# Optimization experiments

Hardware: AMD Instinct MI355X
Metric: run time of the kernel (lower is better)

Reference implementation:

```python
import jax, jax.numpy as jnp
import numpy as np

B, S, D, H, FF = 4, 1024, 1024, 16, 4096
DH = D // H
EPS = 1e-5  # torch LayerNorm default


def _layernorm(x, g, b):
    m = jnp.mean(x, axis=-1, keepdims=True)
    v = jnp.mean((x - m) ** 2, axis=-1, keepdims=True)
    return (x - m) * jax.lax.rsqrt(v + EPS) * g + b


def setup_inputs() -> dict:
    key = jax.random.key(0)
    ks = jax.random.split(key, 8)
    init = lambda k, shape: jax.random.normal(k, shape, jnp.float32) * 0.02
    return {
        "x": jax.random.normal(ks[0], (B, S, D), jnp.float32),
        "Wq": init(ks[1], (D, D)), "bq": jnp.zeros((D,), jnp.float32),
        "Wk": init(ks[2], (D, D)), "bk": jnp.zeros((D,), jnp.float32),
        "Wv": init(ks[3], (D, D)), "bv": jnp.zeros((D,), jnp.float32),
        "Wo": init(ks[4], (D, D)), "bo": jnp.zeros((D,), jnp.float32),
        "ln1_g": jnp.ones((D,), jnp.float32), "ln1_b": jnp.zeros((D,), jnp.float32),
        "W1": init(ks[5], (D, FF)), "b1": jnp.zeros((FF,), jnp.float32),
        "W2": init(ks[6], (FF, D)), "b2": jnp.zeros((D,), jnp.float32),
        "ln2_g": jnp.ones((D,), jnp.float32), "ln2_b": jnp.zeros((D,), jnp.float32),
    }


def reference(x, Wq, bq, Wk, bk, Wv, bv, Wo, bo,
              ln1_g, ln1_b, W1, b1, W2, b2, ln2_g, ln2_b):
    Bx, Sx, _ = x.shape

    def heads(w, b):  # [B,S,D] -> [B,H,S,DH]
        return (x @ w + b).reshape(Bx, Sx, H, DH).transpose(0, 2, 1, 3)

    q, k, v = heads(Wq, bq), heads(Wk, bk), heads(Wv, bv)
    scores = jnp.einsum('bhqd,bhkd->bhqk', q, k) / jnp.sqrt(jnp.float32(DH))
    causal = jnp.tril(jnp.ones((Sx, Sx), bool))
    scores = jnp.where(causal[None, None], scores, jnp.float32(-1e9))
    attn = jax.nn.softmax(scores, axis=-1)           # [B,H,S,S]
    ctx = jnp.einsum('bhqk,bhkd->bqhd', attn, v).reshape(Bx, Sx, D)
    attn_out = ctx @ Wo + bo
    h = _layernorm(x + attn_out, ln1_g, ln1_b)
    ff = jax.nn.relu(h @ W1 + b1) @ W2 + b2
    y = _layernorm(h + ff, ln2_g, ln2_b)
    return (y, attn)
```

## Files before the change

### kernel.cpp

```cpp
#include <hip/hip_runtime.h>
#include <cstdint>


#define T_B 4
#define T_S 1024
#define T_D 1024
#define T_H 16
#define T_DH 64
#define T_FF 4096
#define T_TOK (T_B * T_S)

typedef __attribute__((ext_vector_type(8))) short bf16x8;
typedef __attribute__((ext_vector_type(4))) float f32x4;

__device__ __forceinline__ short f2bf(float f) {
  uint32_t u = __float_as_uint(f);
  u += 0x7FFFu + ((u >> 16) & 1u);
  return (short)(u >> 16);
}

__device__ __forceinline__ float bf2f(short s) {
  return __uint_as_float(((uint32_t)(unsigned short)s) << 16);
}

__device__ __forceinline__ void async_copy16(void* lds, const void* g) {
  __builtin_amdgcn_global_load_lds(
      (__attribute__((address_space(1))) uint32_t*)(uintptr_t)g,
      (__attribute__((address_space(3))) uint32_t*)(uint32_t)(uintptr_t)lds,
      16, 0, 0);
}

__device__ __forceinline__ void stage_ring(char* base, const char* gA0,
                                           const char* gA1, const char* gB0,
                                           const char* gB1, int koffA, int koffB,
                                           int wid) {
  async_copy16(base + (wid << 10), gA0 + koffA);
  async_copy16(base + 4096 + (wid << 10), gA1 + koffA);
  async_copy16(base + 8192 + (wid << 10), gB0 + koffB);
  async_copy16(base + 12288 + (wid << 10), gB1 + koffB);
}

__device__ __forceinline__ void compute32(const char* slot, int wm, int quad,
                                          int r16, int boffB, f32x4 acc[4][4]) {
  const short* As = (const short*)slot;
  bf16x8 av[4], bv[4];
#pragma unroll
  for (int i = 0; i < 4; ++i) {
    av[i] = *(const bf16x8*)(As + ((wm + i * 16 + r16) << 5) + (quad << 3));
    bv[i] = *(const bf16x8*)(slot + 8192 + boffB + (i << 10));
  }
#pragma unroll
  for (int mi = 0; mi < 4; ++mi)
#pragma unroll
    for (int ni = 0; ni < 4; ++ni)
      acc[mi][ni] = __builtin_amdgcn_mfma_f32_16x16x32_bf16(av[mi], bv[ni],
                                                            acc[mi][ni], 0, 0, 0);
}

__device__ __forceinline__ void mfma_loop_ring(
    const short* __restrict__ A, int lda, const char* __restrict__ Bpack,
    int ldbK, int kBase, int kLen, int m0, int n0, char* smem,
    f32x4 acc[4][4]) {
  const int t = threadIdx.x;
  const int lane = t & 63, wid = t >> 6;
  const int wm = (wid >> 1) << 6, wn = (wid & 1) << 6;
  const int quad = lane >> 4, r16 = lane & 15;
  const int boffB = ((wn >> 6) << 12) + (lane << 4);
  const int row0 = t >> 2, cb0 = (t & 3) << 4;
  const char* gA0 = (const char*)A + (((size_t)(m0 + row0) * lda) << 1) + cb0;
  const char* gA1 = gA0 + ((size_t)lda << 7);
  const char* gB0 = Bpack +
      ((size_t)(n0 >> 7) * (ldbK >> 5) + (kBase >> 5)) * 8192 + (t << 4);
  const char* gB1 = gB0 + 4096;

  const f32x4 zf = {0.f, 0.f, 0.f, 0.f};
#pragma unroll
  for (int i = 0; i < 4; ++i)
#pragma unroll
    for (int j = 0; j < 4; ++j) acc[i][j] = zf;

  const int nIter = kLen >> 5;
  stage_ring(smem, gA0, gA1, gB0, gB1, 0, 0, wid);
  stage_ring(smem + 16384, gA0, gA1, gB0, gB1, 64, 8192, wid);
  asm volatile("s_waitcnt vmcnt(4)" ::: "memory");
  __builtin_amdgcn_s_barrier();
  __builtin_amdgcn_sched_barrier(0);

  int cur = 0;
  for (int it = 0; it < nIter; ++it) {
    const int k2 = (it + 2) << 5;
    if (k2 < kLen) {
      int nb = cur + 2;
      if (nb >= 3) nb -= 3;
      stage_ring(smem + nb * 16384, gA0, gA1, gB0, gB1, k2 << 1, k2 << 8, wid);
    }
    compute32(smem + cur * 16384, wm, quad, r16, boffB, acc);
    if (k2 < kLen)
      asm volatile("s_waitcnt vmcnt(4)" ::: "memory");
    else
      asm volatile("s_waitcnt vmcnt(0)" ::: "memory");
    __builtin_amdgcn_s_barrier();
    __builtin_amdgcn_sched_barrier(0);
    ++cur;
    if (cur >= 3) cur -= 3;
  }
}

template <int MODE>
__global__ __launch_bounds__(256) void gemm_dense(
    const short* __restrict__ A, const short* __restrict__ Bw, int K, int N,
    const float* __restrict__ bias0, const float* __restrict__ bias1,
    const float* __restrict__ bias2, short* __restrict__ outb0,
    short* __restrict__ outb1, short* __restrict__ outb2) {
  __shared__ __align__(16) char smem[49152];
  const int m0 = blockIdx.x << 7, n0 = blockIdx.y << 7;
  f32x4 acc[4][4];
  mfma_loop_ring(A, K, (const char*)Bw, K, 0, K, m0, n0, smem, acc);

  const int t = threadIdx.x;
  const int lane = t & 63, wid = t >> 6;
  const int wm = (wid >> 1) << 6, wn = (wid & 1) << 6;
  const int quad = lane >> 4, r16 = lane & 15;

  if constexpr (MODE == 0) {
    const int which = n0 >> 10;
    const float* bias = (which == 0) ? bias0 : (which == 1) ? bias1 : bias2;
    if (which < 2) {
      short* outp = (which == 0) ? outb0 : outb1;
#pragma unroll
      for (int mi = 0; mi < 4; ++mi) {
#pragma unroll
        for (int ni = 0; ni < 4; ++ni) {
          const int col = n0 + wn + ni * 16 + r16;
          const int c10 = col & 1023;
          const float bb = bias[c10];
          const int hh = c10 >> 6, dh = col & 63;
#pragma unroll
          for (int reg = 0; reg < 4; ++reg) {
            const int row = m0 + wm + mi * 16 + quad * 4 + reg;
            const int b = row >> 10, s = row & 1023;
            outp[((((size_t)b * T_H + hh) * T_S) + s) * T_DH + dh] =
                f2bf(acc[mi][ni][reg] + bb);
          }
        }
      }
    } else {
      __syncthreads();
      short* vtile = (short*)smem;
#pragma unroll
      for (int mi = 0; mi < 4; ++mi)
#pragma unroll
        for (int ni = 0; ni < 4; ++ni) {
          const int c = wn + ni * 16 + r16;
          const float bb = bias[(n0 + c) & 1023];
#pragma unroll
          for (int reg = 0; reg < 4; ++reg) {
            const int r = wm + mi * 16 + quad * 4 + reg;
            vtile[c * 136 + r] = f2bf(acc[mi][ni][reg] + bb);
          }
        }
      __syncthreads();
      const int b = m0 >> 10, s0 = m0 & 1023;
      const int c = t >> 1, half = t & 1;
      const int c10 = (n0 + c) & 1023;
      const int hh = c10 >> 6, dh = c10 & 63;
      short* dst = outb2 + (((size_t)b * T_H + hh) * T_DH + dh) * T_S + s0 + half * 64;
      const short* srcl = vtile + c * 136 + half * 64;
#pragma unroll
      for (int j = 0; j < 8; ++j)
        *(bf16x8*)(dst + j * 8) = *(const bf16x8*)(srcl + j * 8);
    }
  } else {
#pragma unroll
    for (int mi = 0; mi < 4; ++mi)
#pragma unroll
      for (int ni = 0; ni < 4; ++ni) {
        const int col = n0 + wn + ni * 16 + r16;
        const float bb = bias0[col];
#pragma unroll
        for (int reg = 0; reg < 4; ++reg) {
          const int row = m0 + wm + mi * 16 + quad * 4 + reg;
          outb0[(size_t)row * N + col] = f2bf(fmaxf(acc[mi][ni][reg] + bb, 0.f));
        }
      }
  }
}

__global__ __launch_bounds__(256) void gemm_splitk(
    const short* __restrict__ A, const short* __restrict__ Bw, int K, int N,
    int kc, float* __restrict__ outp) {
  __shared__ __align__(16) char smem[49152];
  const int m0 = blockIdx.x << 7, n0 = blockIdx.y << 7, z = blockIdx.z;
  f32x4 acc[4][4];
  mfma_loop_ring(A + (size_t)z * kc, K, (const char*)Bw, K, z * kc, kc, m0, n0,
                 smem, acc);
  float* o = outp + (size_t)z * T_TOK * N;
  const int t = threadIdx.x;
  const int lane = t & 63, wid = t >> 6;
  const int wm = (wid >> 1) << 6, wn = (wid & 1) << 6;
  const int quad = lane >> 4, r16 = lane & 15;
#pragma unroll
  for (int mi = 0; mi < 4; ++mi)
#pragma unroll
    for (int ni = 0; ni < 4; ++ni) {
      const int col = n0 + wn + ni * 16 + r16;
#pragma unroll
      for (int reg = 0; reg < 4; ++reg) {
        const int row = m0 + wm + mi * 16 + quad * 4 + reg;
        o[(size_t)row * N + col] = acc[mi][ni][reg];
      }
    }
}

__global__ __launch_bounds__(256) void attn_pass1(
    const short* __restrict__ qg, const short* __restrict__ kg,
    const short* __restrict__ vg, short* __restrict__ ctx,
    float* __restrict__ rsinv_g) {
  const int qb = blockIdx.x;
  const int bh = blockIdx.y;
  const int b = bh >> 4, h = bh & 15;
  const int m0 = qb << 7;
  __shared__ __align__(16) short Es[4 * 128 * 32];
  __shared__ float rsbuf[2][128];
  const int t = threadIdx.x;
  const int lane = t & 63, wid = t >> 6;
  const int quad = lane >> 4, r16 = lane & 15;
  const int wm = (wid >> 1) << 6, wn = (wid & 1) << 6;
  const int pvm = wid << 5;

  const short* Qbh = qg + (size_t)bh * T_S * T_DH;
  const short* Kbh = kg + (size_t)bh * T_S * T_DH;
  const short* Vbh = vg + (size_t)bh * T_DH * T_S;

  bf16x8 qf[4][2];
#pragma unroll
  for (int mi = 0; mi < 4; ++mi)
#pragma unroll
    for (int ksd = 0; ksd < 2; ++ksd)
      qf[mi][ksd] = *(const bf16x8*)(Qbh + (size_t)(m0 + wm + mi * 16 + r16) * T_DH +
                                     ksd * 32 + quad * 8);

  float rs[4][4];
#pragma unroll
  for (int i = 0; i < 4; ++i)
#pragma unroll
    for (int j = 0; j < 4; ++j) rs[i][j] = 0.f;
  const f32x4 zf = {0.f, 0.f, 0.f, 0.f};
  f32x4 accp[2][4];
#pragma unroll
  for (int i = 0; i < 2; ++i)
#pragma unroll
    for (int j = 0; j < 4; ++j) accp[i][j] = zf;

  for (int kt = 0; kt <= qb; ++kt) {
    f32x4 accs[4][4];
#pragma unroll
    for (int i = 0; i < 4; ++i)
#pragma unroll
      for (int j = 0; j < 4; ++j) accs[i][j] = zf;
#pragma unroll
    for (int ksd = 0; ksd < 2; ++ksd) {
      bf16x8 bv[4];
#pragma unroll
      for (int ni = 0; ni < 4; ++ni)
        bv[ni] = *(const bf16x8*)(Kbh + (size_t)(kt * 128 + wn + ni * 16 + r16) * T_DH +
                                  ksd * 32 + quad * 8);
#pragma unroll
      for (int mi = 0; mi < 4; ++mi)
#pragma unroll
        for (int ni = 0; ni < 4; ++ni)
          accs[mi][ni] = __builtin_amdgcn_mfma_f32_16x16x32_bf16(
              qf[mi][ksd], bv[ni], accs[mi][ni], 0, 0, 0);
    }
    __syncthreads();
    const bool diag = (kt == qb);
#pragma unroll
    for (int mi = 0; mi < 4; ++mi) {
#pragma unroll
      for (int ni = 0; ni < 4; ++ni) {
        const int cbase = wn + ni * 16;
        const int kse = cbase >> 5;
        const int sin = (cbase & 31) + r16;
        short* ep = Es + kse * 4096 + (wm + mi * 16 + quad * 4) * 32 + sin;
        const int colw = cbase + r16;
#pragma unroll
        for (int reg = 0; reg < 4; ++reg) {
          float e = __expf(accs[mi][ni][reg] * 0.125f);
          if (diag && colw > (wm + mi * 16 + quad * 4 + reg)) e = 0.f;
          ep[reg * 32] = f2bf(e);
          rs[mi][reg] += e;
        }
      }
    }
    __syncthreads();
#pragma unroll
    for (int ks = 0; ks < 4; ++ks) {
      bf16x8 av[2], bvv[4];
#pragma unroll
      for (int i = 0; i < 2; ++i)
        av[i] = *(const bf16x8*)(Es + ks * 4096 + (pvm + i * 16 + r16) * 32 + quad * 8);
#pragma unroll
      for (int ni = 0; ni < 4; ++ni)
        bvv[ni] = *(const bf16x8*)(Vbh + (size_t)(ni * 16 + r16) * T_S + kt * 128 +
                                   ks * 32 + quad * 8);
#pragma unroll
      for (int i = 0; i < 2; ++i)
#pragma unroll
        for (int ni = 0; ni < 4; ++ni)
          accp[i][ni] = __builtin_amdgcn_mfma_f32_16x16x32_bf16(av[i], bvv[ni],
                                                                accp[i][ni], 0, 0, 0);
    }
  }

#pragma unroll
  for (int mi = 0; mi < 4; ++mi)
#pragma unroll
    for (int reg = 0; reg < 4; ++reg) {
#pragma unroll
      for (int d = 1; d < 16; d <<= 1)
        rs[mi][reg] += __shfl_xor(rs[mi][reg], d, 64);
    }
  if (r16 == 0) {
#pragma unroll
    for (int mi = 0; mi < 4; ++mi)
#pragma unroll
      for (int reg = 0; reg < 4; ++reg)
        rsbuf[wid & 1][wm + mi * 16 + quad * 4 + reg] = rs[mi][reg];
  }
  __syncthreads();
  if (t < 128) {
    const float iv = 1.f / (rsbuf[0][t] + rsbuf[1][t]);
    rsbuf[0][t] = iv;
    rsinv_g[(size_t)bh * T_S + m0 + t] = iv;
  }
  __syncthreads();
#pragma unroll
  for (int i = 0; i < 2; ++i)
#pragma unroll
    for (int ni = 0; ni < 4; ++ni) {
#pragma unroll
      for (int reg = 0; reg < 4; ++reg) {
        const int row = pvm + i * 16 + quad * 4 + reg;
        const float iv = rsbuf[0][row];
        ctx[((size_t)b * T_S + m0 + row) * T_D + h * 64 + ni * 16 + r16] =
            f2bf(accp[i][ni][reg] * iv);
      }
    }
}

__global__ __launch_bounds__(256) void attn_pass2(
    const short* __restrict__ qg, const short* __restrict__ kg,
    const float* __restrict__ rsinv_g, float* __restrict__ attn) {
  const int qb = blockIdx.x, kt = blockIdx.y, bh = blockIdx.z;
  float* out = attn + ((size_t)bh * T_S + qb * 128) * T_S + kt * 128;
  const int t = threadIdx.x;
  if (kt > qb) {
    const float4 z4 = {0.f, 0.f, 0.f, 0.f};
#pragma unroll
    for (int j = 0; j < 16; ++j) {
      const int id = t + j * 256;
      ((float4*)(out + (size_t)(id >> 5) * T_S))[id & 31] = z4;
    }
    return;
  }
  const int lane = t & 63, wid = t >> 6;
  const int quad = lane >> 4, r16 = lane & 15;
  const int wm = (wid >> 1) << 6, wn = (wid & 1) << 6;
  const short* Qbh = qg + (size_t)bh * T_S * T_DH;
  const short* Kbh = kg + (size_t)bh * T_S * T_DH;
  const f32x4 zf = {0.f, 0.f, 0.f, 0.f};
  f32x4 accs[4][4];
#pragma unroll
  for (int i = 0; i < 4; ++i)
#pragma unroll
    for (int j = 0; j < 4; ++j) accs[i][j] = zf;
#pragma unroll
  for (int ksd = 0; ksd < 2; ++ksd) {
    bf16x8 aq[4], bv[4];
#pragma unroll
    for (int mi = 0; mi < 4; ++mi)
      aq[mi] = *(const bf16x8*)(Qbh + (size_t)(qb * 128 + wm + mi * 16 + r16) * T_DH +
                                ksd * 32 + quad * 8);
#pragma unroll
    for (int ni = 0; ni < 4; ++ni)
      bv[ni] = *(const bf16x8*)(Kbh + (size_t)(kt * 128 + wn + ni * 16 + r16) * T_DH +
                                ksd * 32 + quad * 8);
#pragma unroll
    for (int mi = 0; mi < 4; ++mi)
#pragma unroll
      for (int ni = 0; ni < 4; ++ni)
        accs[mi][ni] = __builtin_amdgcn_mfma_f32_16x16x32_bf16(aq[mi], bv[ni],
                                                               accs[mi][ni], 0, 0, 0);
  }
  const bool diag = (kt == qb);
#pragma unroll
  for (int mi = 0; mi < 4; ++mi)
#pragma unroll
    for (int ni = 0; ni < 4; ++ni) {
      const int col = wn + ni * 16 + r16;
#pragma unroll
      for (int reg = 0; reg < 4; ++reg) {
        const int rowt = wm + mi * 16 + quad * 4 + reg;
        const float iv = rsinv_g[(size_t)bh * T_S + qb * 128 + rowt];
        float e = __expf(accs[mi][ni][reg] * 0.125f) * iv;
        if (diag && col > rowt) e = 0.f;
        out[(size_t)rowt * T_S + col] = e;
      }
    }
}

__global__ __launch_bounds__(256) void ln_multi(
    const float* __restrict__ a32, const short* __restrict__ a16,
    const float* __restrict__ parts, int nparts, const float* __restrict__ bias,
    const float* __restrict__ g, const float* __restrict__ be,
    float* __restrict__ outf, short* __restrict__ outb) {
  const int row = blockIdx.x;
  const int t = threadIdx.x;
  float4 x;
  if (a32 != nullptr) {
    x = ((const float4*)(a32 + (size_t)row * T_D))[t];
  } else {
    const short4 s4 = ((const short4*)(a16 + (size_t)row * T_D))[t];
    x.x = bf2f(s4.x); x.y = bf2f(s4.y); x.z = bf2f(s4.z); x.w = bf2f(s4.w);
  }
  const float4 bv = ((const float4*)bias)[t];
  x.x += bv.x; x.y += bv.y; x.z += bv.z; x.w += bv.w;
  for (int p = 0; p < nparts; ++p) {
    const float4 v =
        ((const float4*)(parts + (size_t)p * T_TOK * T_D + (size_t)row * T_D))[t];
    x.x += v.x; x.y += v.y; x.z += v.z; x.w += v.w;
  }
  float sum = x.x + x.y + x.z + x.w;
  float sq = x.x * x.x + x.y * x.y + x.z * x.z + x.w * x.w;
  __shared__ float reds[4], redq[4];
  const int lane = t & 63, wid = t >> 6;
#pragma unroll
  for (int o = 32; o > 0; o >>= 1) {
    sum += __shfl_down(sum, o, 64);
    sq += __shfl_down(sq, o, 64);
  }
  if (lane == 0) { reds[wid] = sum; redq[wid] = sq; }
  __syncthreads();
  sum = reds[0] + reds[1] + reds[2] + reds[3];
  sq = redq[0] + redq[1] + redq[2] + redq[3];
  const float mean = sum * (1.f / T_D);
  const float var = sq * (1.f / T_D) - mean * mean;
  const float rstd = rsqrtf(var + 1e-5f);
  const float4 gg = ((const float4*)g)[t];
  const float4 bb = ((const float4*)be)[t];
  float4 y;
  y.x = (x.x - mean) * rstd * gg.x + bb.x;
  y.y = (x.y - mean) * rstd * gg.y + bb.y;
  y.z = (x.z - mean) * rstd * gg.z + bb.z;
  y.w = (x.w - mean) * rstd * gg.w + bb.w;
  if (outf != nullptr) ((float4*)(outf + (size_t)row * T_D))[t] = y;
  if (outb != nullptr) {
    short4 o4;
    o4.x = f2bf(y.x); o4.y = f2bf(y.y); o4.z = f2bf(y.z); o4.w = f2bf(y.w);
    ((short4*)(outb + (size_t)row * T_D))[t] = o4;
  }
}

__global__ __launch_bounds__(256) void prep_kernel(
    const float* __restrict__ x, short* __restrict__ xb,
    const float* __restrict__ Wq, const float* __restrict__ Wk,
    const float* __restrict__ Wv, const float* __restrict__ Wo,
    const float* __restrict__ W1, const float* __restrict__ W2,
    short* __restrict__ Wqkv_t, short* __restrict__ Wo_t,
    short* __restrict__ W1_t, short* __restrict__ W2_t) {
  int id = blockIdx.x;
  const int t = threadIdx.x;
  if (id < 4096) {
    const int i = id * 256 + t;
    const float4 v = ((const float4*)x)[i];
    short4 o;
    o.x = f2bf(v.x); o.y = f2bf(v.y); o.z = f2bf(v.z); o.w = f2bf(v.w);
    ((short4*)xb)[i] = o;
    return;
  }
  id -= 4096;
  const float* src;
  short* dst;
  int R, C;
  if (id < 1024) { src = Wq; dst = Wqkv_t; R = 1024; C = 1024; }
  else if (id < 2048) { id -= 1024; src = Wk; dst = Wqkv_t + 1024 * 1024; R = 1024; C = 1024; }
  else if (id < 3072) { id -= 2048; src = Wv; dst = Wqkv_t + 2 * 1024 * 1024; R = 1024; C = 1024; }
  else if (id < 4096) { id -= 3072; src = Wo; dst = Wo_t; R = 1024; C = 1024; }
  else if (id < 8192) { id -= 4096; src = W1; dst = W1_t; R = 1024; C = 4096; }
  else { id -= 8192; src = W2; dst = W2_t; R = 4096; C = 1024; }
  const int tilesC = C >> 5;
  const int r0 = (id / tilesC) << 5, c0 = (id % tilesC) << 5;
  __shared__ float tile[32][33];
  const int tx = t & 31, ty = t >> 5;
#pragma unroll
  for (int j = 0; j < 4; ++j)
    tile[ty + j * 8][tx] = src[(size_t)(r0 + ty + j * 8) * C + c0 + tx];
  __syncthreads();
  if (t < 128) {
    const int b = t >> 2, c = t & 3;
    bf16x8 v8;
#pragma unroll
    for (int j = 0; j < 8; ++j) v8[j] = f2bf(tile[c * 8 + j][b]);
    const int p = c0 >> 7, h = (c0 >> 6) & 1;
    const int g = ((c0 & 63) >> 4) + (b >> 4), r = b & 15;
    char* dp = (char*)dst + ((size_t)p * (R >> 5) + (r0 >> 5)) * 8192 +
               h * 4096 + g * 1024 + c * 256 + r * 16;
    *(bf16x8*)dp = v8;
  }
}

extern "C" void kernel_launch(void* const* d_in, const int* in_sizes, int n_in,
                              void* d_out, int out_size, void* d_ws,
                              size_t ws_size, hipStream_t stream) {
  const float* x = (const float*)d_in[0];
  const float* Wq = (const float*)d_in[1];
  const float* bq = (const float*)d_in[2];
  const float* Wk = (const float*)d_in[3];
  const float* bk = (const float*)d_in[4];
  const float* Wv = (const float*)d_in[5];
  const float* bv = (const float*)d_in[6];
  const float* Wo = (const float*)d_in[7];
  const float* bo = (const float*)d_in[8];
  const float* ln1g = (const float*)d_in[9];
  const float* ln1b = (const float*)d_in[10];
  const float* W1 = (const float*)d_in[11];
  const float* b1 = (const float*)d_in[12];
  const float* W2 = (const float*)d_in[13];
  const float* b2 = (const float*)d_in[14];
  const float* ln2g = (const float*)d_in[15];
  const float* ln2b = (const float*)d_in[16];
  (void)in_sizes; (void)n_in; (void)out_size; (void)ws_size;

  float* y_out = (float*)d_out;
  float* attn = (float*)d_out + (size_t)T_TOK * T_D;

  char* w = (char*)d_ws;
  size_t off = 0;
  auto alloc = [&](size_t bytes) -> void* {
    void* p = w + off;
    off += (bytes + 255) & ~(size_t)255;
    return p;
  };
  short* xb     = (short*)alloc((size_t)T_TOK * T_D * 2);
  short* Wqkv_t = (short*)alloc((size_t)3 * T_D * T_D * 2);
  short* Wo_t   = (short*)alloc((size_t)T_D * T_D * 2);
  short* W1_t   = (short*)alloc((size_t)T_FF * T_D * 2);
  short* W2_t   = (short*)alloc((size_t)T_D * T_FF * 2);
  short* qb_    = (short*)alloc((size_t)T_TOK * T_D * 2);
  short* kb_    = (short*)alloc((size_t)T_TOK * T_D * 2);
  short* vtb    = (short*)alloc((size_t)T_TOK * T_D * 2);
  short* ctx    = (short*)alloc((size_t)T_TOK * T_D * 2);
  short* hb     = (short*)alloc((size_t)T_TOK * T_D * 2);
  short* ff1    = (short*)alloc((size_t)T_TOK * T_FF * 2);
  float* rsinv  = (float*)alloc((size_t)T_H * T_B * T_S * 4);
  float* woP    = (float*)alloc((size_t)2 * T_TOK * T_D * 4);
  float* ffP    = (float*)alloc((size_t)2 * T_TOK * T_D * 4);

  prep_kernel<<<dim3(16384), dim3(256), 0, stream>>>(
      x, xb, Wq, Wk, Wv, Wo, W1, W2, Wqkv_t, Wo_t, W1_t, W2_t);

  gemm_dense<0><<<dim3(32, 24), dim3(256), 0, stream>>>(
      xb, Wqkv_t, T_D, 3072, bq, bk, bv, qb_, kb_, vtb);
  attn_pass1<<<dim3(8, 64), dim3(256), 0, stream>>>(qb_, kb_, vtb, ctx, rsinv);
  attn_pass2<<<dim3(8, 8, 64), dim3(256), 0, stream>>>(qb_, kb_, rsinv, attn);

  gemm_splitk<<<dim3(32, 8, 2), dim3(256), 0, stream>>>(ctx, Wo_t, T_D, T_D, 512, woP);
  ln_multi<<<dim3(4096), dim3(256), 0, stream>>>(x, nullptr, woP, 2, bo, ln1g,
                                                 ln1b, nullptr, hb);

  gemm_dense<2><<<dim3(32, 32), dim3(256), 0, stream>>>(
      hb, W1_t, T_D, T_FF, b1, nullptr, nullptr, ff1, nullptr, nullptr);
  gemm_splitk<<<dim3(32, 8, 2), dim3(256), 0, stream>>>(ff1, W2_t, T_FF, T_D, 2048, ffP);
  ln_multi<<<dim3(4096), dim3(256), 0, stream>>>(nullptr, hb, ffP, 2, b2, ln2g,
                                                 ln2b, y_out, nullptr);
}
```

Before: 616.8 us.

## Co-schedule attention probability writes with FF2 split-K GEMM in one launch

Removes the standalone attn_pass2 launch and merges its blocks into the FF2 split-K GEMM launch: the first 512 blocks run the GEMM, the remaining 4096 write the attention probability tiles. The aim is to let the bandwidth-heavy attn matrix writes overlap with the compute-bound FF2 GEMM, and to fill the GPU tail of the 512-block GEMM. The cost is that every block reserves the GEMM's 48KB shared memory, including pass2 blocks that need none, which limits occupancy. Register pressure also becomes the maximum of the two code paths.

```diff
diff --git a/kernel.cpp b/kernel.cpp
--- a/kernel.cpp
+++ b/kernel.cpp
@@ -106,6 +106,95 @@
   }
 }
 
+__device__ __forceinline__ void splitk_body(int m0, int n0, int z,
+                                            const short* __restrict__ A,
+                                            const short* __restrict__ Bw, int K,
+                                            int N, int kc,
+                                            float* __restrict__ outp,
+                                            char* smem) {
+  f32x4 acc[4][4];
+  mfma_loop_ring(A + (size_t)z * kc, K, (const char*)Bw, K, z * kc, kc, m0, n0,
+                 smem, acc);
+  float* o = outp + (size_t)z * T_TOK * N;
+  const int t = threadIdx.x;
+  const int lane = t & 63, wid = t >> 6;
+  const int wm = (wid >> 1) << 6, wn = (wid & 1) << 6;
+  const int quad = lane >> 4, r16 = lane & 15;
+#pragma unroll
+  for (int mi = 0; mi < 4; ++mi)
+#pragma unroll
+    for (int ni = 0; ni < 4; ++ni) {
+      const int col = n0 + wn + ni * 16 + r16;
+#pragma unroll
+      for (int reg = 0; reg < 4; ++reg) {
+        const int row = m0 + wm + mi * 16 + quad * 4 + reg;
+        o[(size_t)row * N + col] = acc[mi][ni][reg];
+      }
+    }
+}
+
+__device__ __forceinline__ void pass2_body(int qb, int kt, int bh,
+                                           const short* __restrict__ qg,
+                                           const short* __restrict__ kg,
+                                           const float* __restrict__ rsinv_g,
+                                           float* __restrict__ attn) {
+  float* out = attn + ((size_t)bh * T_S + qb * 128) * T_S + kt * 128;
+  const int t = threadIdx.x;
+  if (kt > qb) {
+    const float4 z4 = {0.f, 0.f, 0.f, 0.f};
+#pragma unroll
+    for (int j = 0; j < 16; ++j) {
+      const int id = t + j * 256;
+      ((float4*)(out + (size_t)(id >> 5) * T_S))[id & 31] = z4;
+    }
+    return;
+  }
+  const int lane = t & 63, wid = t >> 6;
+  const int quad = lane >> 4, r16 = lane & 15;
+  const int wm = (wid >> 1) << 6, wn = (wid & 1) << 6;
+  const short* Qbh = qg + (size_t)bh * T_S * T_DH;
+  const short* Kbh = kg + (size_t)bh * T_S * T_DH;
+  const f32x4 zf = {0.f, 0.f, 0.f, 0.f};
+  f32x4 accs[4][4];
+#pragma unroll
+  for (int i = 0; i < 4; ++i)
+#pragma unroll
+    for (int j = 0; j < 4; ++j) accs[i][j] = zf;
+#pragma unroll
+  for (int ksd = 0; ksd < 2; ++ksd) {
+    bf16x8 aq[4], bv[4];
+#pragma unroll
+    for (int mi = 0; mi < 4; ++mi)
+      aq[mi] = *(const bf16x8*)(Qbh + (size_t)(qb * 128 + wm + mi * 16 + r16) * T_DH +
+                                ksd * 32 + quad * 8);
+#pragma unroll
+    for (int ni = 0; ni < 4; ++ni)
+      bv[ni] = *(const bf16x8*)(Kbh + (size_t)(kt * 128 + wn + ni * 16 + r16) * T_DH +
+                                ksd * 32 + quad * 8);
+#pragma unroll
+    for (int mi = 0; mi < 4; ++mi)
+#pragma unroll
+      for (int ni = 0; ni < 4; ++ni)
+        accs[mi][ni] = __builtin_amdgcn_mfma_f32_16x16x32_bf16(aq[mi], bv[ni],
+                                                               accs[mi][ni], 0, 0, 0);
+  }
+  const bool diag = (kt == qb);
+#pragma unroll
+  for (int mi = 0; mi < 4; ++mi)
+#pragma unroll
+    for (int ni = 0; ni < 4; ++ni) {
+      const int col = wn + ni * 16 + r16;
+#pragma unroll
+      for (int reg = 0; reg < 4; ++reg) {
+        const int rowt = wm + mi * 16 + quad * 4 + reg;
+        const float iv = rsinv_g[(size_t)bh * T_S + qb * 128 + rowt];
+        float e = __expf(accs[mi][ni][reg] * 0.125f) * iv;
+        if (diag && col > rowt) e = 0.f;
+        out[(size_t)rowt * T_S + col] = e;
+      }
+    }
+}
+
 template <int MODE>
 __global__ __launch_bounds__(256) void gemm_dense(
     const short* __restrict__ A, const short* __restrict__ Bw, int K, int N,
@@ -190,26 +279,24 @@
     const short* __restrict__ A, const short* __restrict__ Bw, int K, int N,
     int kc, float* __restrict__ outp) {
   __shared__ __align__(16) char smem[49152];
-  const int m0 = blockIdx.x << 7, n0 = blockIdx.y << 7, z = blockIdx.z;
-  f32x4 acc[4][4];
-  mfma_loop_ring(A + (size_t)z * kc, K, (const char*)Bw, K, z * kc, kc, m0, n0,
-                 smem, acc);
-  float* o = outp + (size_t)z * T_TOK * N;
-  const int t = threadIdx.x;
-  const int lane = t & 63, wid = t >> 6;
-  const int wm = (wid >> 1) << 6, wn = (wid & 1) << 6;
-  const int quad = lane >> 4, r16 = lane & 15;
-#pragma unroll
-  for (int mi = 0; mi < 4; ++mi)
-#pragma unroll
-    for (int ni = 0; ni < 4; ++ni) {
-      const int col = n0 + wn + ni * 16 + r16;
-#pragma unroll
-      for (int reg = 0; reg < 4; ++reg) {
-        const int row = m0 + wm + mi * 16 + quad * 4 + reg;
-        o[(size_t)row * N + col] = acc[mi][ni][reg];
-      }
-    }
+  splitk_body(blockIdx.x << 7, blockIdx.y << 7, blockIdx.z, A, Bw, K, N, kc,
+              outp, smem);
+}
+
+__global__ __launch_bounds__(256) void ff2_attn_fused(
+    const short* __restrict__ A, const short* __restrict__ Bw, int K, int N,
+    int kc, float* __restrict__ outp, const short* __restrict__ qg,
+    const short* __restrict__ kg, const float* __restrict__ rsinv_g,
+    float* __restrict__ attn) {
+  __shared__ __align__(16) char smem[49152];
+  const int bx = blockIdx.x;
+  if (bx < 512) {
+    splitk_body((bx & 31) << 7, ((bx >> 5) & 7) << 7, bx >> 8, A, Bw, K, N, kc,
+                outp, smem);
+  } else {
+    const int id = bx - 512;
+    pass2_body(id & 7, (id >> 3) & 7, id >> 6, qg, kg, rsinv_g, attn);
+  }
 }
 
 __global__ __launch_bounds__(256) void attn_pass1(
@@ -344,67 +431,6 @@
         const float iv = rsbuf[0][row];
         ctx[((size_t)b * T_S + m0 + row) * T_D + h * 64 + ni * 16 + r16] =
             f2bf(accp[i][ni][reg] * iv);
-      }
-    }
-}
-
-__global__ __launch_bounds__(256) void attn_pass2(
-    const short* __restrict__ qg, const short* __restrict__ kg,
-    const float* __restrict__ rsinv_g, float* __restrict__ attn) {
-  const int qb = blockIdx.x, kt = blockIdx.y, bh = blockIdx.z;
-  float* out = attn + ((size_t)bh * T_S + qb * 128) * T_S + kt * 128;
-  const int t = threadIdx.x;
-  if (kt > qb) {
-    const float4 z4 = {0.f, 0.f, 0.f, 0.f};
-#pragma unroll
-    for (int j = 0; j < 16; ++j) {
-      const int id = t + j * 256;
-      ((float4*)(out + (size_t)(id >> 5) * T_S))[id & 31] = z4;
-    }
-    return;
-  }
-  const int lane = t & 63, wid = t >> 6;
-  const int quad = lane >> 4, r16 = lane & 15;
-  const int wm = (wid >> 1) << 6, wn = (wid & 1) << 6;
-  const short* Qbh = qg + (size_t)bh * T_S * T_DH;
-  const short* Kbh = kg + (size_t)bh * T_S * T_DH;
-  const f32x4 zf = {0.f, 0.f, 0.f, 0.f};
-  f32x4 accs[4][4];
-#pragma unroll
-  for (int i = 0; i < 4; ++i)
-#pragma unroll
-    for (int j = 0; j < 4; ++j) accs[i][j] = zf;
-#pragma unroll
-  for (int ksd = 0; ksd < 2; ++ksd) {
-    bf16x8 aq[4], bv[4];
-#pragma unroll
-    for (int mi = 0; mi < 4; ++mi)
-      aq[mi] = *(const bf16x8*)(Qbh + (size_t)(qb * 128 + wm + mi * 16 + r16) * T_DH +
-                                ksd * 32 + quad * 8);
-#pragma unroll
-    for (int ni = 0; ni < 4; ++ni)
-      bv[ni] = *(const bf16x8*)(Kbh + (size_t)(kt * 128 + wn + ni * 16 + r16) * T_DH +
-                                ksd * 32 + quad * 8);
-#pragma unroll
-    for (int mi = 0; mi < 4; ++mi)
-#pragma unroll
-      for (int ni = 0; ni < 4; ++ni)
-        accs[mi][ni] = __builtin_amdgcn_mfma_f32_16x16x32_bf16(aq[mi], bv[ni],
-                                                               accs[mi][ni], 0, 0, 0);
-  }
-  const bool diag = (kt == qb);
-#pragma unroll
-  for (int mi = 0; mi < 4; ++mi)
-#pragma unroll
-    for (int ni = 0; ni < 4; ++ni) {
-      const int col = wn + ni * 16 + r16;
-#pragma unroll
-      for (int reg = 0; reg < 4; ++reg) {
-        const int rowt = wm + mi * 16 + quad * 4 + reg;
-        const float iv = rsinv_g[(size_t)bh * T_S + qb * 128 + rowt];
-        float e = __expf(accs[mi][ni][reg] * 0.125f) * iv;
-        if (diag && col > rowt) e = 0.f;
-        out[(size_t)rowt * T_S + col] = e;
       }
     }
 }
@@ -562,7 +588,6 @@
   gemm_dense<0><<<dim3(32, 24), dim3(256), 0, stream>>>(
       xb, Wqkv_t, T_D, 3072, bq, bk, bv, qb_, kb_, vtb);
   attn_pass1<<<dim3(8, 64), dim3(256), 0, stream>>>(qb_, kb_, vtb, ctx, rsinv);
-  attn_pass2<<<dim3(8, 8, 64), dim3(256), 0, stream>>>(qb_, kb_, rsinv, attn);
 
   gemm_splitk<<<dim3(32, 8, 2), dim3(256), 0, stream>>>(ctx, Wo_t, T_D, T_D, 512, woP);
   ln_multi<<<dim3(4096), dim3(256), 0, stream>>>(x, nullptr, woP, 2, bo, ln1g,
@@ -570,7 +595,8 @@
 
   gemm_dense<2><<<dim3(32, 32), dim3(256), 0, stream>>>(
       hb, W1_t, T_D, T_FF, b1, nullptr, nullptr, ff1, nullptr, nullptr);
-  gemm_splitk<<<dim3(32, 8, 2), dim3(256), 0, stream>>>(ff1, W2_t, T_FF, T_D, 2048, ffP);
+  ff2_attn_fused<<<dim3(4608), dim3(256), 0, stream>>>(
+      ff1, W2_t, T_FF, T_D, 2048, ffP, qb_, kb_, rsinv, attn);
   ln_multi<<<dim3(4096), dim3(256), 0, stream>>>(nullptr, hb, ffP, 2, b2, ln2g,
                                                  ln2b, y_out, nullptr);
 }
```

New measurement: 609.0 us. Within noise of the previous version (-1.3%).
